# Kernel optimization log

Hardware: AMD Instinct MI355X
Metric: run time of the kernel (lower is better)

## Reference

```python
import jax, jax.numpy as jnp
import numpy as np
import math

IN_FEATURES = 1024
OUT_FEATURES = 1024
N_BANK = 8192
N_LAYER = 12
N_EMBD = 1024


def setup_inputs() -> dict:
    key = jax.random.key(0)
    kq, kk, kv = jax.random.split(key, 3)
    q = jax.random.normal(kq, (4, 2048, IN_FEATURES), dtype=jnp.float32)
    k = 0.02 * jax.random.normal(kk, (N_BANK, IN_FEATURES), dtype=jnp.float32)
    v_std = 2.0 / N_LAYER / math.sqrt(N_EMBD)
    v = v_std * jax.random.normal(kv, (N_BANK, OUT_FEATURES), dtype=jnp.float32)
    return {"q": q, "k": k, "v": v}


def reference(q, k, v):
    # scores: [B, T, N]
    scores = jnp.einsum("btd,nd->btn", q, k)
    # row-wise L2 normalization, scaled by sqrt(N), then exact (erf) GELU
    sqrt_n = jnp.sqrt(jnp.asarray(scores.shape[-1], scores.dtype))
    norm = jnp.linalg.norm(scores, axis=-1, keepdims=True)
    gated = jax.nn.gelu(scores / norm * sqrt_n, approximate=False)
    # out: [B, T, out_features]
    return jnp.einsum("btn,no->bto", gated, v)
```

## Files before the change

kernel.cpp:

```cpp
#include <hip/hip_runtime.h>
#include <hip/hip_bf16.h>
#include <math.h>


#define MROWS 8192
#define DIN   1024
#define NBANK 8192
#define DOUT  1024

typedef float  f32x4  __attribute__((ext_vector_type(4)));
typedef __bf16 bf16x8 __attribute__((ext_vector_type(8)));

__device__ __forceinline__ float bf2f(unsigned short u) {
  union { unsigned int i; float f; } x; x.i = ((unsigned int)u) << 16; return x.f;
}
__device__ __forceinline__ unsigned short f2bf(float f) {
  union { float f; unsigned int i; } x; x.f = f;
  unsigned int u = x.i;
  unsigned int r = (u + 0x7fffu + ((u >> 16) & 1u)) >> 16;
  return (unsigned short)r;
}

__global__ void cvt_kernel(const float* __restrict__ src,
                           unsigned short* __restrict__ dst, int n) {
  int i = (blockIdx.x * 256 + threadIdx.x) * 4;
  if (i >= n) return;
  float4 vv = *(const float4*)(src + i);
  ushort4 o;
  o.x = f2bf(vv.x); o.y = f2bf(vv.y); o.z = f2bf(vv.z); o.w = f2bf(vv.w);
  *(ushort4*)(dst + i) = o;
}

__global__ void transpose_cvt_kernel(const float* __restrict__ src,
                                     unsigned short* __restrict__ dst,
                                     int R, int C) {
  __shared__ float tile[32][33];
  int c0 = blockIdx.x * 32, r0 = blockIdx.y * 32;
  for (int i = threadIdx.y; i < 32; i += 8)
    tile[i][threadIdx.x] = src[(size_t)(r0 + i) * C + c0 + threadIdx.x];
  __syncthreads();
  for (int i = threadIdx.y; i < 32; i += 8)
    dst[(size_t)(c0 + i) * R + r0 + threadIdx.x] = f2bf(tile[threadIdx.x][i]);
}

__global__ void zero_f32_kernel(float* __restrict__ p, int n4) {
  int i = blockIdx.x * 256 + threadIdx.x;
  if (i < n4) ((float4*)p)[i] = make_float4(0.f, 0.f, 0.f, 0.f);
}


__device__ __forceinline__ void stage_half(const unsigned short* src, int ld,
                                           unsigned short* dstbase, int tid) {
  __builtin_amdgcn_global_load_lds(
      (const __attribute__((address_space(1))) unsigned int*)src,
      (__attribute__((address_space(3))) unsigned int*)(dstbase + tid * 8), 16, 0, 0);
  __builtin_amdgcn_global_load_lds(
      (const __attribute__((address_space(1))) unsigned int*)(src + (size_t)128 * ld),
      (__attribute__((address_space(3))) unsigned int*)(dstbase + 4096 + tid * 8), 16,
      0, 0);
}

__device__ __forceinline__ void read4(const unsigned short* base, bf16x8 f[4]) {
#pragma unroll
  for (int i = 0; i < 4; ++i) f[i] = *(const bf16x8*)(base + i * 512);
}

__device__ __forceinline__ void mfma16(const bf16x8 a[4], const bf16x8 b[4],
                                       f32x4 (&acc)[8][4], int mh) {
#pragma unroll
  for (int m = 0; m < 4; ++m)
#pragma unroll
    for (int n = 0; n < 4; ++n)
      acc[mh * 4 + m][n] = __builtin_amdgcn_mfma_f32_16x16x32_bf16(
          a[m], b[n], acc[mh * 4 + m][n], 0, 0, 0);
}

__device__ __forceinline__ void gemm_core(const unsigned short* __restrict__ Ap,
                                          const unsigned short* __restrict__ Bp,
                                          int lda, int ldb, int nkt,
                                          unsigned short* As, unsigned short* Bs,
                                          f32x4 (&acc)[8][4]) {
  const int tid  = threadIdx.x;
  const int lane = tid & 63;
  const int wm   = (tid >> 6) >> 2;
  const int wn   = (tid >> 6) & 3;
  const int quad = lane >> 4;
  const int l16  = lane & 15;
  const int aoff = (wm * 128 + l16) * 32 + quad * 8;
  const int boff = (wn * 64 + l16) * 32 + quad * 8;

  const unsigned short* Ag = Ap + (size_t)(tid >> 2) * lda + (tid & 3) * 8;
  const unsigned short* Bg = Bp + (size_t)(tid >> 2) * ldb + (tid & 3) * 8;

#pragma unroll
  for (int i = 0; i < 8; ++i)
#pragma unroll
    for (int j = 0; j < 4; ++j) {
      f32x4 z = {0.f, 0.f, 0.f, 0.f};
      acc[i][j] = z;
    }

  stage_half(Ag, lda, As, tid);
  stage_half(Bg, ldb, Bs, tid);
  stage_half(Ag + 32, lda, As + 8192, tid);
  stage_half(Bg + 32, ldb, Bs + 8192, tid);
  asm volatile("s_waitcnt vmcnt(4)" ::: "memory");
  __builtin_amdgcn_s_barrier();

  for (int kt = 0; kt < nkt; ++kt) {
    const int cur = kt & 1, nx = cur ^ 1;
    const unsigned short* Ab = As + cur * 16384;
    const unsigned short* Bb = Bs + cur * 16384;
    unsigned short* Asn = As + nx * 16384;
    unsigned short* Bsn = Bs + nx * 16384;
    const bool pf = (kt + 1 < nkt);
    const int knext = (kt + 1) * 64;
    bf16x8 a[4], b[4];

    read4(Ab + aoff, a);
    read4(Bb + boff, b);
    if (pf) stage_half(Ag + knext, lda, Asn, tid);
    __builtin_amdgcn_s_barrier();
    asm volatile("s_waitcnt lgkmcnt(0)" ::: "memory");
    __builtin_amdgcn_sched_barrier(0);
    __builtin_amdgcn_s_setprio(1);
    mfma16(a, b, acc, 0);
    __builtin_amdgcn_s_setprio(0);
    __builtin_amdgcn_s_barrier();

    read4(Ab + aoff + 2048, a);
    if (pf) stage_half(Bg + knext, ldb, Bsn, tid);
    __builtin_amdgcn_s_barrier();
    asm volatile("s_waitcnt lgkmcnt(0)" ::: "memory");
    __builtin_amdgcn_sched_barrier(0);
    __builtin_amdgcn_s_setprio(1);
    mfma16(a, b, acc, 1);
    __builtin_amdgcn_s_setprio(0);
    if (pf)
      asm volatile("s_waitcnt vmcnt(4)" ::: "memory");
    else
      asm volatile("s_waitcnt vmcnt(0)" ::: "memory");
    __builtin_amdgcn_s_barrier();

    read4(Ab + 8192 + aoff + 2048, a);
    read4(Bb + 8192 + boff, b);
    if (pf) stage_half(Ag + knext + 32, lda, Asn + 8192, tid);
    __builtin_amdgcn_s_barrier();
    asm volatile("s_waitcnt lgkmcnt(0)" ::: "memory");
    __builtin_amdgcn_sched_barrier(0);
    __builtin_amdgcn_s_setprio(1);
    mfma16(a, b, acc, 1);
    __builtin_amdgcn_s_setprio(0);
    __builtin_amdgcn_s_barrier();

    read4(Ab + 8192 + aoff, a);
    if (pf) stage_half(Bg + knext + 32, ldb, Bsn + 8192, tid);
    __builtin_amdgcn_s_barrier();
    asm volatile("s_waitcnt lgkmcnt(0)" ::: "memory");
    __builtin_amdgcn_sched_barrier(0);
    __builtin_amdgcn_s_setprio(1);
    mfma16(a, b, acc, 0);
    __builtin_amdgcn_s_setprio(0);
    if (pf) asm volatile("s_waitcnt vmcnt(4)" ::: "memory");
    __builtin_amdgcn_s_barrier();
  }
}

__global__ __launch_bounds__(512) void gemm1_kernel(
    const unsigned short* __restrict__ A, const unsigned short* __restrict__ B,
    unsigned short* __restrict__ C, float* __restrict__ sumsq) {
  __shared__ unsigned short As[2 * 16384];
  __shared__ unsigned short Bs[2 * 16384];

  const int flat = blockIdx.y * gridDim.x + blockIdx.x;
  const int nwg  = gridDim.x * gridDim.y;
  const int swz  = (flat & 7) * (nwg >> 3) + (flat >> 3);
  const size_t m0 = (size_t)(swz / gridDim.x) * 256;
  const size_t n0 = (size_t)(swz % gridDim.x) * 256;

  f32x4 acc[8][4];
  gemm_core(A + m0 * DIN, B + n0 * DIN, DIN, DIN, DIN / 64, As, Bs, acc);

  const int tid  = threadIdx.x;
  const int lane = tid & 63;
  const int wm   = (tid >> 6) >> 2;
  const int wn   = (tid >> 6) & 3;
  const int quad = lane >> 4;
  const int l16  = lane & 15;

#pragma unroll
  for (int mf = 0; mf < 8; ++mf)
#pragma unroll
    for (int r = 0; r < 4; ++r) {
      size_t row = m0 + wm * 128 + mf * 16 + quad * 4 + r;
      float s = 0.f;
#pragma unroll
      for (int nf = 0; nf < 4; ++nf) {
        float val = acc[mf][nf][r];
        s += val * val;
        C[row * (size_t)NBANK + n0 + wn * 64 + nf * 16 + l16] = f2bf(val);
      }
      s += __shfl_xor(s, 1);
      s += __shfl_xor(s, 2);
      s += __shfl_xor(s, 4);
      s += __shfl_xor(s, 8);
      if (l16 == 0) atomicAdd(&sumsq[row], s);
    }
}

__global__ void gelu_kernel(unsigned short* __restrict__ S,
                            const float* __restrict__ sumsq) {
  const size_t total = (size_t)MROWS * NBANK / 8;
  for (size_t u = (size_t)blockIdx.x * 256 + threadIdx.x; u < total;
       u += (size_t)gridDim.x * 256) {
    size_t idx = u * 8;
    int row = (int)(idx >> 13);
    float sc = sqrtf((float)NBANK / sumsq[row]);
    uint4 vv = *(const uint4*)(S + idx);
    unsigned int w[4] = {vv.x, vv.y, vv.z, vv.w};
#pragma unroll
    for (int e = 0; e < 4; e++) {
      float x0 = bf2f((unsigned short)(w[e] & 0xffffu)) * sc;
      float x1 = bf2f((unsigned short)(w[e] >> 16)) * sc;
      float g0 = 0.5f * x0 * (1.0f + erff(x0 * 0.70710678118654752f));
      float g1 = 0.5f * x1 * (1.0f + erff(x1 * 0.70710678118654752f));
      w[e] = (unsigned int)f2bf(g0) | ((unsigned int)f2bf(g1) << 16);
    }
    uint4 o; o.x = w[0]; o.y = w[1]; o.z = w[2]; o.w = w[3];
    *(uint4*)(S + idx) = o;
  }
}

__global__ __launch_bounds__(512) void gemm2_kernel(
    const unsigned short* __restrict__ A,
    const unsigned short* __restrict__ B,
    float* __restrict__ C) {
  __shared__ unsigned short As[2 * 16384];
  __shared__ unsigned short Bs[2 * 16384];

  const int flat = blockIdx.y * gridDim.x + blockIdx.x;
  const int nwg  = gridDim.x * gridDim.y;
  const int swz  = (flat & 7) * (nwg >> 3) + (flat >> 3);
  const size_t m0 = (size_t)(swz / gridDim.x) * 256;
  const size_t n0 = (size_t)(swz % gridDim.x) * 256;
  const int kbase = blockIdx.z * (NBANK / 2);

  f32x4 acc[8][4];
  gemm_core(A + m0 * (size_t)NBANK + kbase, B + n0 * (size_t)NBANK + kbase, NBANK,
            NBANK, (NBANK / 2) / 64, As, Bs, acc);

  const int tid  = threadIdx.x;
  const int lane = tid & 63;
  const int wm   = (tid >> 6) >> 2;
  const int wn   = (tid >> 6) & 3;
  const int quad = lane >> 4;
  const int l16  = lane & 15;

#pragma unroll
  for (int mf = 0; mf < 8; ++mf)
#pragma unroll
    for (int nf = 0; nf < 4; ++nf)
#pragma unroll
      for (int r = 0; r < 4; ++r) {
        size_t row = m0 + wm * 128 + mf * 16 + quad * 4 + r;
        size_t col = n0 + wn * 64 + nf * 16 + l16;
        atomicAdd(&C[row * (size_t)DOUT + col], acc[mf][nf][r]);
      }
}

extern "C" void kernel_launch(void* const* d_in, const int* in_sizes, int n_in,
                              void* d_out, int out_size, void* d_ws, size_t ws_size,
                              hipStream_t stream) {
  const float* q = (const float*)d_in[0];
  const float* k = (const float*)d_in[1];
  const float* v = (const float*)d_in[2];
  float* out = (float*)d_out;

  char* ws = (char*)d_ws;
  const size_t MB = 1024ull * 1024ull;
  unsigned short* qb     = (unsigned short*)(ws);
  unsigned short* kb     = (unsigned short*)(ws + 16 * MB);
  unsigned short* vbT    = (unsigned short*)(ws + 32 * MB);
  unsigned short* scores = (unsigned short*)(ws + 48 * MB);
  float*          scale  = (float*)(ws + 176 * MB);

  const int nqk = MROWS * DIN;

  zero_f32_kernel<<<(MROWS * DOUT / 4 + 255) / 256, 256, 0, stream>>>(out,
                                                                      MROWS * DOUT / 4);
  zero_f32_kernel<<<(MROWS / 4 + 255) / 256, 256, 0, stream>>>(scale, MROWS / 4);

  cvt_kernel<<<nqk / 1024, 256, 0, stream>>>(q, qb, nqk);
  cvt_kernel<<<nqk / 1024, 256, 0, stream>>>(k, kb, nqk);
  transpose_cvt_kernel<<<dim3(DOUT / 32, NBANK / 32), dim3(32, 8), 0, stream>>>(
      v, vbT, NBANK, DOUT);

  gemm1_kernel<<<dim3(NBANK / 256, MROWS / 256), 512, 0, stream>>>(qb, kb, scores,
                                                                   scale);

  gelu_kernel<<<4096, 256, 0, stream>>>(scores, scale);

  gemm2_kernel<<<dim3(DOUT / 256, MROWS / 256, 2), 512, 0, stream>>>(scores, vbT, out);
}
```

Measured before the change: 575.4 us.

## Replace split-K atomic gemm2 with 128x128 tiled direct-store kernel

Rewrites the second GEMM to use 128x128 tiles with 256 threads, a single 32-wide K stage loaded via global_load_lds, and no split-K. Output is written directly instead of by atomicAdd, which also removes the zeroing pass over the output. In exchange it loses double buffering and the larger 256x256 tile reuse, so each K step stalls on loads behind two barriers, and the 16x16x32 MFMA per-wave work is smaller.

Result: faster. 544.3 us (-5.4%).

```diff
diff --git a/kernel.cpp b/kernel.cpp
--- a/kernel.cpp
+++ b/kernel.cpp
@@ -231,40 +231,90 @@
   }
 }
 
-__global__ __launch_bounds__(512) void gemm2_kernel(
+__global__ __launch_bounds__(256, 4) void gemm2_kernel(
     const unsigned short* __restrict__ A,
     const unsigned short* __restrict__ B,
     float* __restrict__ C) {
-  __shared__ unsigned short As[2 * 16384];
-  __shared__ unsigned short Bs[2 * 16384];
+  __shared__ unsigned short As[128 * 32];
+  __shared__ unsigned short Bs[128 * 32];
+  const int K = NBANK, ldc = DOUT;
+
+  const int tid  = threadIdx.x;
+  const int lane = tid & 63;
+  const int wave = tid >> 6;
+  const int wm   = (wave >> 1) * 64;
+  const int wn   = (wave & 1) * 64;
+  const int quad = lane >> 4;
+  const int l16  = lane & 15;
 
   const int flat = blockIdx.y * gridDim.x + blockIdx.x;
   const int nwg  = gridDim.x * gridDim.y;
   const int swz  = (flat & 7) * (nwg >> 3) + (flat >> 3);
-  const size_t m0 = (size_t)(swz / gridDim.x) * 256;
-  const size_t n0 = (size_t)(swz % gridDim.x) * 256;
-  const int kbase = blockIdx.z * (NBANK / 2);
-
-  f32x4 acc[8][4];
-  gemm_core(A + m0 * (size_t)NBANK + kbase, B + n0 * (size_t)NBANK + kbase, NBANK,
-            NBANK, (NBANK / 2) / 64, As, Bs, acc);
-
-  const int tid  = threadIdx.x;
-  const int lane = tid & 63;
-  const int wm   = (tid >> 6) >> 2;
-  const int wn   = (tid >> 6) & 3;
-  const int quad = lane >> 4;
-  const int l16  = lane & 15;
-
-#pragma unroll
-  for (int mf = 0; mf < 8; ++mf)
-#pragma unroll
-    for (int nf = 0; nf < 4; ++nf)
-#pragma unroll
-      for (int r = 0; r < 4; ++r) {
-        size_t row = m0 + wm * 128 + mf * 16 + quad * 4 + r;
-        size_t col = n0 + wn * 64 + nf * 16 + l16;
-        atomicAdd(&C[row * (size_t)DOUT + col], acc[mf][nf][r]);
+  const size_t m0 = (size_t)(swz / gridDim.x) * 128;
+  const size_t n0 = (size_t)(swz % gridDim.x) * 128;
+
+  const int srow = tid >> 2;
+  const int scol = (tid & 3) * 8;
+  const unsigned short* Ag0 = A + (m0 + srow) * (size_t)K + scol;
+  const unsigned short* Ag1 = A + (m0 + srow + 64) * (size_t)K + scol;
+  const unsigned short* Bg0 = B + (n0 + srow) * (size_t)K + scol;
+  const unsigned short* Bg1 = B + (n0 + srow + 64) * (size_t)K + scol;
+
+  unsigned short* AsW0 = As + tid * 8;
+  unsigned short* AsW1 = As + 64 * 32 + tid * 8;
+  unsigned short* BsW0 = Bs + tid * 8;
+  unsigned short* BsW1 = Bs + 64 * 32 + tid * 8;
+
+  const unsigned short* ArP = As + (wm + l16) * 32 + quad * 8;
+  const unsigned short* BrP = Bs + (wn + l16) * 32 + quad * 8;
+
+  f32x4 acc[4][4];
+#pragma unroll
+  for (int i = 0; i < 4; i++)
+#pragma unroll
+    for (int j = 0; j < 4; j++) {
+      f32x4 z = {0.f, 0.f, 0.f, 0.f};
+      acc[i][j] = z;
+    }
+
+  for (int k0 = 0; k0 < K; k0 += 32) {
+    __builtin_amdgcn_global_load_lds(
+        (const __attribute__((address_space(1))) unsigned int*)(Ag0 + k0),
+        (__attribute__((address_space(3))) unsigned int*)AsW0, 16, 0, 0);
+    __builtin_amdgcn_global_load_lds(
+        (const __attribute__((address_space(1))) unsigned int*)(Ag1 + k0),
+        (__attribute__((address_space(3))) unsigned int*)AsW1, 16, 0, 0);
+    __builtin_amdgcn_global_load_lds(
+        (const __attribute__((address_space(1))) unsigned int*)(Bg0 + k0),
+        (__attribute__((address_space(3))) unsigned int*)BsW0, 16, 0, 0);
+    __builtin_amdgcn_global_load_lds(
+        (const __attribute__((address_space(1))) unsigned int*)(Bg1 + k0),
+        (__attribute__((address_space(3))) unsigned int*)BsW1, 16, 0, 0);
+    __syncthreads();
+
+    bf16x8 af[4], bfr[4];
+#pragma unroll
+    for (int i = 0; i < 4; i++) af[i] = *(const bf16x8*)(ArP + i * 16 * 32);
+#pragma unroll
+    for (int j = 0; j < 4; j++) bfr[j] = *(const bf16x8*)(BrP + j * 16 * 32);
+#pragma unroll
+    for (int i = 0; i < 4; i++)
+#pragma unroll
+      for (int j = 0; j < 4; j++)
+        acc[i][j] = __builtin_amdgcn_mfma_f32_16x16x32_bf16(af[i], bfr[j],
+                                                            acc[i][j], 0, 0, 0);
+    __syncthreads();
+  }
+
+#pragma unroll
+  for (int i = 0; i < 4; i++)
+#pragma unroll
+    for (int j = 0; j < 4; j++)
+#pragma unroll
+      for (int r = 0; r < 4; r++) {
+        size_t row = m0 + wm + i * 16 + quad * 4 + r;
+        size_t col = n0 + wn + j * 16 + l16;
+        C[row * (size_t)ldc + col] = acc[i][j][r];
       }
 }
 
@@ -286,8 +336,6 @@
 
   const int nqk = MROWS * DIN;
 
-  zero_f32_kernel<<<(MROWS * DOUT / 4 + 255) / 256, 256, 0, stream>>>(out,
-                                                                      MROWS * DOUT / 4);
   zero_f32_kernel<<<(MROWS / 4 + 255) / 256, 256, 0, stream>>>(scale, MROWS / 4);
 
   cvt_kernel<<<nqk / 1024, 256, 0, stream>>>(q, qb, nqk);
@@ -300,5 +348,5 @@
 
   gelu_kernel<<<4096, 256, 0, stream>>>(scores, scale);
 
-  gemm2_kernel<<<dim3(DOUT / 256, MROWS / 256, 2), 512, 0, stream>>>(scores, vbT, out);
-}
+  gemm2_kernel<<<dim3(DOUT / 128, MROWS / 128), 256, 0, stream>>>(scores, vbT, out);
+}
```
